# Optimization experiments

Hardware: AMD Instinct MI355X
Metric: run time of the kernel (lower is better)

The kernel has to match this reference:

```python
import jax, jax.numpy as jnp
import numpy as np

EMB = 384
HEADS = 6
QDIM = 64
DFF = 4 * EMB
EPS = 1e-5


def layer_norm(x, g, b):
    mu = jnp.mean(x, axis=-1, keepdims=True)
    var = jnp.mean((x - mu) ** 2, axis=-1, keepdims=True)
    return (x - mu) * jax.lax.rsqrt(var + EPS) * g + b


def setup_inputs() -> dict:
    key = jax.random.key(0)
    ks = jax.random.split(key, 12)
    s = EMB ** -0.5
    return {
        "x": jax.random.normal(ks[0], (32, 512, EMB), dtype=jnp.float32),
        "Wq": jax.random.normal(ks[1], (EMB, EMB), dtype=jnp.float32) * s,
        "Wk": jax.random.normal(ks[2], (EMB, EMB), dtype=jnp.float32) * s,
        "Wv": jax.random.normal(ks[3], (EMB, EMB), dtype=jnp.float32) * s,
        "Wp": jax.random.normal(ks[4], (EMB, EMB), dtype=jnp.float32) * s,
        "bp": jnp.zeros((EMB,), dtype=jnp.float32),
        "g1": jnp.ones((EMB,), dtype=jnp.float32),
        "b1": jnp.zeros((EMB,), dtype=jnp.float32),
        "g2": jnp.ones((EMB,), dtype=jnp.float32),
        "b2": jnp.zeros((EMB,), dtype=jnp.float32),
        "W1": jax.random.normal(ks[5], (EMB, DFF), dtype=jnp.float32) * s,
        "bf1": jnp.zeros((DFF,), dtype=jnp.float32),
        "W2": jax.random.normal(ks[6], (DFF, EMB), dtype=jnp.float32) * (DFF ** -0.5),
        "bf2": jnp.zeros((EMB,), dtype=jnp.float32),
    }


def reference(x, Wq, Wk, Wv, Wp, bp, g1, b1, g2, b2, W1, bf1, W2, bf2):
    B, T, C = x.shape
    # --- self-attention on ln1(x) ---
    h = layer_norm(x, g1, b1)
    q = (h @ Wq).reshape(B, T, HEADS, QDIM).transpose(0, 2, 1, 3)  # [B,H,T,D]
    k = (h @ Wk).reshape(B, T, HEADS, QDIM).transpose(0, 2, 1, 3)
    v = (h @ Wv).reshape(B, T, HEADS, QDIM).transpose(0, 2, 1, 3)
    aff = jnp.einsum('bhtd,bhsd->bhts', q, k) * (QDIM ** -0.5)  # [B,H,T,T]
    causal = jnp.tril(jnp.ones((T, T), dtype=bool))
    aff = jnp.where(causal, aff, -jnp.inf)
    aff = jax.nn.softmax(aff, axis=-1)
    o = jnp.einsum('bhts,bhsd->bhtd', aff, v)
    o = o.transpose(0, 2, 1, 3).reshape(B, T, C)
    x = x + (o @ Wp + bp)
    # --- feed-forward on ln2(x) ---
    h2 = layer_norm(x, g2, b2)
    ff = jax.nn.relu(h2 @ W1 + bf1) @ W2 + bf2
    return x + ff
```

## Files before the change

kernel.cpp:

```cpp
#include <hip/hip_runtime.h>
#include <cstdint>
#include <cstddef>

#define DEVINL __device__ __forceinline__

typedef short short8 __attribute__((ext_vector_type(8)));
typedef float f32x4 __attribute__((ext_vector_type(4)));
typedef unsigned short ushort;
typedef ushort u16x8 __attribute__((ext_vector_type(8)));
typedef ushort u16x4 __attribute__((ext_vector_type(4)));

DEVINL float bf2f(ushort u) {
  union { unsigned int i; float f; } v; v.i = ((unsigned int)u) << 16; return v.f;
}
DEVINL ushort f2bf(float f) {
  union { float f; unsigned int i; } v; v.f = f;
  unsigned int u = v.i;
  unsigned int r = u + 0x7fffu + ((u >> 16) & 1u);
  return (ushort)(r >> 16);
}

DEVINL void gl2lds16(const ushort* g, ushort* l) {
  __builtin_amdgcn_global_load_lds(
      (const __attribute__((address_space(1))) void*)g,
      (__attribute__((address_space(3))) void*)l, 16, 0, 0);
}

__global__ void transpose4_k(const float* __restrict__ i0, const float* __restrict__ i1,
                             const float* __restrict__ i2, const float* __restrict__ i3,
                             ushort* __restrict__ o0, ushort* __restrict__ o1,
                             ushort* __restrict__ o2, ushort* __restrict__ o3) {
  __shared__ float tile[32][33];
  int z = blockIdx.z;
  const float* in = (z == 0) ? i0 : (z == 1) ? i1 : (z == 2) ? i2 : i3;
  ushort* out = (z == 0) ? o0 : (z == 1) ? o1 : (z == 2) ? o2 : o3;
  int bx = blockIdx.x, by = blockIdx.y;
  int tx = threadIdx.x, ty = threadIdx.y;
  int x = bx * 32 + tx;
#pragma unroll
  for (int i = 0; i < 4; i++) {
    int y = by * 32 + ty + i * 8;
    tile[ty + i * 8][tx] = in[(size_t)y * 384 + x];
  }
  __syncthreads();
  int x2 = by * 32 + tx;
#pragma unroll
  for (int i = 0; i < 4; i++) {
    int y2 = bx * 32 + ty + i * 8;
    out[(size_t)y2 * 384 + x2] = f2bf(tile[tx][ty + i * 8]);
  }
}

__global__ void transpose_k(const float* __restrict__ in, ushort* __restrict__ out,
                            int R, int C) {
  __shared__ float tile[32][33];
  int bx = blockIdx.x, by = blockIdx.y;
  int tx = threadIdx.x, ty = threadIdx.y;
  int x = bx * 32 + tx;
#pragma unroll
  for (int i = 0; i < 4; i++) {
    int y = by * 32 + ty + i * 8;
    tile[ty + i * 8][tx] = in[(size_t)y * C + x];
  }
  __syncthreads();
  int x2 = by * 32 + tx;
#pragma unroll
  for (int i = 0; i < 4; i++) {
    int y2 = bx * 32 + ty + i * 8;
    out[(size_t)y2 * R + x2] = f2bf(tile[tx][ty + i * 8]);
  }
}

__global__ __launch_bounds__(256) void ln_k(const float* __restrict__ x,
                                            const float* __restrict__ g,
                                            const float* __restrict__ b,
                                            ushort* __restrict__ out) {
  int wave = threadIdx.x >> 6;
  int lane = threadIdx.x & 63;
  int row = blockIdx.x * 4 + wave;
  const float* xr = x + (size_t)row * 384;
  float v[6];
#pragma unroll
  for (int j = 0; j < 3; j++) {
    float2 p = *(const float2*)(xr + lane * 2 + j * 128);
    v[2 * j] = p.x;
    v[2 * j + 1] = p.y;
  }
  float s = v[0] + v[1] + v[2] + v[3] + v[4] + v[5];
#pragma unroll
  for (int off = 32; off; off >>= 1) s += __shfl_xor(s, off);
  float mu = s * (1.0f / 384.0f);
  float s2 = 0.f;
#pragma unroll
  for (int j = 0; j < 6; j++) { float d = v[j] - mu; s2 += d * d; }
#pragma unroll
  for (int off = 32; off; off >>= 1) s2 += __shfl_xor(s2, off);
  float rs = rsqrtf(s2 * (1.0f / 384.0f) + 1e-5f);
  ushort* orow = out + (size_t)row * 384;
#pragma unroll
  for (int j = 0; j < 3; j++) {
    int c = lane * 2 + j * 128;
    float2 pg = *(const float2*)(g + c);
    float2 pb = *(const float2*)(b + c);
    float y0 = (v[2 * j] - mu) * rs * pg.x + pb.x;
    float y1 = (v[2 * j + 1] - mu) * rs * pg.y + pb.y;
    uint32_t po = (uint32_t)f2bf(y0) | ((uint32_t)f2bf(y1) << 16);
    *(uint32_t*)(orow + c) = po;
  }
}

template <int MODE, int TN>
__global__ __launch_bounds__(256) void gemm_k(
    const ushort* __restrict__ A, int K,
    const ushort* __restrict__ WTa, const ushort* __restrict__ WTb,
    const ushort* __restrict__ WTc,
    const float* __restrict__ bias, const float* residf,
    ushort* __restrict__ outa, ushort* __restrict__ outb,
    ushort* __restrict__ outc, float* outf) {
  constexpr int NJ = TN / 32;
  __shared__ __align__(16) ushort As[128 * 32];
  __shared__ __align__(16) ushort Bs[TN * 32];
  int tid = threadIdx.x;
  int lane = tid & 63, wave = tid >> 6;
  int wm = wave & 1, wn = wave >> 1;
  int q4 = lane >> 4, ln16 = lane & 15;
  int rowBase = blockIdx.x * 128;
  int colBase = blockIdx.y * TN;

  const ushort* WT;
  if (MODE == 0) {
    int z = blockIdx.z;
    WT = (z == 0) ? WTa : (z == 1) ? WTb : WTc;
  } else {
    WT = WTa;
  }

  f32x4 acc[4][NJ];
#pragma unroll
  for (int i = 0; i < 4; i++)
#pragma unroll
    for (int j = 0; j < NJ; j++) acc[i][j] = (f32x4){0.f, 0.f, 0.f, 0.f};

  int lr = lane >> 2;
  int chunk = (lane & 3) ^ (lr & 3);
  int rslot = (q4 ^ (ln16 & 3)) << 3;

  for (int kb = 0; kb < K; kb += 32) {
#pragma unroll
    for (int h = 0; h < 128; h += 64) {
      int base = wave * 16 + h;
      gl2lds16(&A[(size_t)(rowBase + base + lr) * K + kb + chunk * 8], &As[base * 32]);
    }
#pragma unroll
    for (int h = 0; h < TN; h += 64) {
      int base = wave * 16 + h;
      gl2lds16(&WT[(size_t)(colBase + base + lr) * K + kb + chunk * 8], &Bs[base * 32]);
    }
    __syncthreads();
    short8 af[4], bfr[NJ];
#pragma unroll
    for (int i = 0; i < 4; i++) {
      int ar = wm * 64 + i * 16 + ln16;
      af[i] = *(const short8*)&As[ar * 32 + rslot];
    }
#pragma unroll
    for (int j = 0; j < NJ; j++) {
      int br = wn * (TN / 2) + j * 16 + ln16;
      bfr[j] = *(const short8*)&Bs[br * 32 + rslot];
    }
#pragma unroll
    for (int i = 0; i < 4; i++)
#pragma unroll
      for (int j = 0; j < NJ; j++)
        acc[i][j] = __builtin_amdgcn_mfma_f32_16x16x32_bf16(af[i], bfr[j], acc[i][j], 0, 0, 0);
    __syncthreads();
  }

#pragma unroll
  for (int i = 0; i < 4; i++) {
#pragma unroll
    for (int j = 0; j < NJ; j++) {
      int row0 = rowBase + wm * 64 + i * 16 + q4 * 4;
      int col = colBase + wn * (TN / 2) + j * 16 + ln16;
      if (MODE == 0) {
        int z = blockIdx.z;
        if (z < 2) {
          ushort* o = (z == 0) ? outa : outb;
#pragma unroll
          for (int r = 0; r < 4; r++) {
            int row = row0 + r;
            int bb = row >> 9, t = row & 511, h = col >> 6, d = col & 63;
            o[(((size_t)(bb * 6 + h) * 512) + t) * 64 + d] = f2bf(acc[i][j][r]);
          }
        } else {
          int bb = row0 >> 9, t0 = row0 & 511, h = col >> 6, d = col & 63;
          u16x4 pk = {f2bf(acc[i][j][0]), f2bf(acc[i][j][1]), f2bf(acc[i][j][2]),
                      f2bf(acc[i][j][3])};
          *(u16x4*)&outc[(((size_t)(bb * 6 + h) * 64) + d) * 512 + t0] = pk;
        }
      } else if (MODE == 1) {
        float bcol = bias[col];
#pragma unroll
        for (int r = 0; r < 4; r++) {
          size_t idx = (size_t)(row0 + r) * 384 + col;
          outf[idx] = acc[i][j][r] + bcol + residf[idx];
        }
      } else {
        float bcol = bias[col];
#pragma unroll
        for (int r = 0; r < 4; r++) {
          size_t idx = (size_t)(row0 + r) * 1536 + col;
          float vv = acc[i][j][r] + bcol;
          outa[idx] = f2bf(vv > 0.f ? vv : 0.f);
        }
      }
    }
  }
}

__global__ __launch_bounds__(256) void attn_k(const ushort* __restrict__ qg,
                                              const ushort* __restrict__ kg,
                                              const ushort* __restrict__ vtg,
                                              ushort* __restrict__ outg) {
  __shared__ ushort Ks[64][88];
  __shared__ ushort VTs[64][88];
  __shared__ ushort Pw[4][16][88];
  int tid = threadIdx.x, lane = tid & 63, wave = tid >> 6;
  int qb = blockIdx.x;
  int bh = blockIdx.y;
  int quad = lane >> 4, ln16 = lane & 15;
  int q0 = qb * 64 + wave * 16;
  int t_row = q0 + ln16;

  const ushort* qp = qg + (size_t)bh * 512 * 64;
  const ushort* kp = kg + (size_t)bh * 512 * 64;
  const ushort* vp = vtg + (size_t)bh * 64 * 512;

  short8 bq0 = *(const short8*)&qp[(size_t)t_row * 64 + quad * 8];
  short8 bq1 = *(const short8*)&qp[(size_t)t_row * 64 + 32 + quad * 8];

  f32x4 O[4];
#pragma unroll
  for (int dt = 0; dt < 4; dt++) O[dt] = (f32x4){0.f, 0.f, 0.f, 0.f};
  float m_ = -3.0e38f, l_ = 0.f;

  const float SC = 0.125f * 1.44269504088896f;

  for (int s0 = 0; s0 <= qb * 64; s0 += 64) {
    {
      int r = tid >> 2;
      int c0 = (tid & 3) * 8;
#pragma unroll
      for (int p = 0; p < 2; p++) {
        int c = c0 + p * 32;
        *(u16x8*)&Ks[r][c] = *(const u16x8*)&kp[(size_t)(s0 + r) * 64 + c];
        *(u16x8*)&VTs[r][c] = *(const u16x8*)&vp[(size_t)r * 512 + s0 + c];
      }
    }
    __syncthreads();

    f32x4 St[4];
#pragma unroll
    for (int kt = 0; kt < 4; kt++) {
      short8 a0 = *(const short8*)&Ks[kt * 16 + ln16][quad * 8];
      short8 a1 = *(const short8*)&Ks[kt * 16 + ln16][32 + quad * 8];
      f32x4 z = (f32x4){0.f, 0.f, 0.f, 0.f};
      z = __builtin_amdgcn_mfma_f32_16x16x32_bf16(a0, bq0, z, 0, 0, 0);
      z = __builtin_amdgcn_mfma_f32_16x16x32_bf16(a1, bq1, z, 0, 0, 0);
      St[kt] = z;
    }
#pragma unroll
    for (int kt = 0; kt < 4; kt++)
#pragma unroll
      for (int r = 0; r < 4; r++) {
        int s_abs = s0 + kt * 16 + quad * 4 + r;
        float vv = St[kt][r] * SC;
        St[kt][r] = (s_abs <= t_row) ? vv : -3.0e38f;
      }
    float vm = St[0][0];
#pragma unroll
    for (int kt = 0; kt < 4; kt++)
#pragma unroll
      for (int r = 0; r < 4; r++) vm = fmaxf(vm, St[kt][r]);
    vm = fmaxf(vm, __shfl_xor(vm, 16));
    vm = fmaxf(vm, __shfl_xor(vm, 32));
    float mn = fmaxf(m_, vm);
    float alpha = exp2f(m_ - mn);
    m_ = mn;
    float ps = 0.f;
#pragma unroll
    for (int kt = 0; kt < 4; kt++)
#pragma unroll
      for (int r = 0; r < 4; r++) {
        float p = exp2f(St[kt][r] - mn);
        St[kt][r] = p;
        ps += p;
      }
    ps += __shfl_xor(ps, 16);
    ps += __shfl_xor(ps, 32);
    l_ = l_ * alpha + ps;
#pragma unroll
    for (int dt = 0; dt < 4; dt++)
#pragma unroll
      for (int r = 0; r < 4; r++) O[dt][r] *= alpha;

#pragma unroll
    for (int kt = 0; kt < 4; kt++) {
      u16x4 pk = {f2bf(St[kt][0]), f2bf(St[kt][1]), f2bf(St[kt][2]), f2bf(St[kt][3])};
      *(u16x4*)&Pw[wave][ln16][kt * 16 + quad * 4] = pk;
    }
    asm volatile("" ::: "memory");
    union { u16x8 u; short8 s; } p0, p1;
    p0.u = *(const u16x8*)&Pw[wave][ln16][quad * 8];
    p1.u = *(const u16x8*)&Pw[wave][ln16][32 + quad * 8];
#pragma unroll
    for (int dt = 0; dt < 4; dt++) {
      short8 v0 = *(const short8*)&VTs[dt * 16 + ln16][quad * 8];
      short8 v1 = *(const short8*)&VTs[dt * 16 + ln16][32 + quad * 8];
      O[dt] = __builtin_amdgcn_mfma_f32_16x16x32_bf16(v0, p0.s, O[dt], 0, 0, 0);
      O[dt] = __builtin_amdgcn_mfma_f32_16x16x32_bf16(v1, p1.s, O[dt], 0, 0, 0);
    }
    __syncthreads();
  }

  float inv = 1.0f / l_;
  int b = bh / 6, h = bh % 6;
  size_t rowbase = ((size_t)(b * 512) + t_row) * 384 + h * 64;
#pragma unroll
  for (int dt = 0; dt < 4; dt++) {
    u16x4 pk = {f2bf(O[dt][0] * inv), f2bf(O[dt][1] * inv), f2bf(O[dt][2] * inv),
                f2bf(O[dt][3] * inv)};
    *(u16x4*)&outg[rowbase + dt * 16 + quad * 4] = pk;
  }
}

extern "C" void kernel_launch(void* const* d_in, const int* in_sizes, int n_in,
                              void* d_out, int out_size, void* d_ws, size_t ws_size,
                              hipStream_t stream) {
  const float* x = (const float*)d_in[0];
  const float* Wq = (const float*)d_in[1];
  const float* Wk = (const float*)d_in[2];
  const float* Wv = (const float*)d_in[3];
  const float* Wp = (const float*)d_in[4];
  const float* bp = (const float*)d_in[5];
  const float* g1 = (const float*)d_in[6];
  const float* b1 = (const float*)d_in[7];
  const float* g2 = (const float*)d_in[8];
  const float* b2 = (const float*)d_in[9];
  const float* W1 = (const float*)d_in[10];
  const float* bf1 = (const float*)d_in[11];
  const float* W2 = (const float*)d_in[12];
  const float* bf2 = (const float*)d_in[13];
  float* outp = (float*)d_out;

  char* ws = (char*)d_ws;
  size_t off = 0;
  auto alloc = [&](size_t elems) {
    ushort* p = (ushort*)(ws + off);
    off += elems * 2;
    return p;
  };
  ushort* WqT = alloc((size_t)384 * 384);
  ushort* WkT = alloc((size_t)384 * 384);
  ushort* WvT = alloc((size_t)384 * 384);
  ushort* WpT = alloc((size_t)384 * 384);
  ushort* W1T = alloc((size_t)384 * 1536);
  ushort* W2T = alloc((size_t)1536 * 384);
  ushort* bufq = alloc((size_t)16384 * 384);
  ushort* m1 = alloc((size_t)16384 * 1536);
  ushort* h1_attn = m1;
  ushort* bufk = m1 + (size_t)16384 * 384;
  ushort* vT = m1 + (size_t)2 * 16384 * 384;

  dim3 tb(32, 8);
  transpose4_k<<<dim3(12, 12, 4), tb, 0, stream>>>(Wq, Wk, Wv, Wp, WqT, WkT, WvT, WpT);
  transpose_k<<<dim3(48, 12), tb, 0, stream>>>(W1, W1T, 384, 1536);
  transpose_k<<<dim3(12, 48), tb, 0, stream>>>(W2, W2T, 1536, 384);

  ln_k<<<4096, 256, 0, stream>>>(x, g1, b1, h1_attn);
  gemm_k<0, 128><<<dim3(128, 3, 3), 256, 0, stream>>>(
      h1_attn, 384, WqT, WkT, WvT, nullptr, nullptr, bufq, bufk, vT, nullptr);
  attn_k<<<dim3(8, 192), 256, 0, stream>>>(bufq, bufk, vT, h1_attn);
  gemm_k<1, 64><<<dim3(128, 6), 256, 0, stream>>>(
      h1_attn, 384, WpT, nullptr, nullptr, bp, x, nullptr, nullptr, nullptr, outp);
  ln_k<<<4096, 256, 0, stream>>>(outp, g2, b2, bufq);
  gemm_k<2, 128><<<dim3(128, 12), 256, 0, stream>>>(
      bufq, 384, W1T, nullptr, nullptr, bf1, nullptr, m1, nullptr, nullptr, nullptr);
  gemm_k<1, 64><<<dim3(128, 6), 256, 0, stream>>>(
      m1, 1536, W2T, nullptr, nullptr, bf2, outp, nullptr, nullptr, nullptr, outp);
}
```

Baseline: 280.8 us.

## Pair causal query tiles per block and map heads to XCDs for balance

Each attention block now handles two query tiles, lo=pr and hi=7-pr, so every block does the same total causal work. The K/V tiles loaded into LDS are shared between both tiles, which halves K/V staging for the low tile. The grid is flattened to 768 blocks, and block indices are mapped so that all blocks for a given batch-head land on the same XCD, aiming for L2 reuse of K/V. The cost is higher register pressure from two accumulator sets and half as many blocks.

```diff
diff --git a/kernel.cpp b/kernel.cpp
--- a/kernel.cpp
+++ b/kernel.cpp
@@ -226,47 +226,44 @@
   __shared__ ushort VTs[64][88];
   __shared__ ushort Pw[4][16][88];
   int tid = threadIdx.x, lane = tid & 63, wave = tid >> 6;
-  int qb = blockIdx.x;
-  int bh = blockIdx.y;
+  int l = blockIdx.x;
+  int xcd = l & 7, m = l >> 3;
+  int bh = xcd * 24 + (m >> 2);
+  int pr = m & 3;
+  int lo = pr, hi = 7 - pr;
   int quad = lane >> 4, ln16 = lane & 15;
-  int q0 = qb * 64 + wave * 16;
-  int t_row = q0 + ln16;
 
   const ushort* qp = qg + (size_t)bh * 512 * 64;
   const ushort* kp = kg + (size_t)bh * 512 * 64;
   const ushort* vp = vtg + (size_t)bh * 64 * 512;
 
-  short8 bq0 = *(const short8*)&qp[(size_t)t_row * 64 + quad * 8];
-  short8 bq1 = *(const short8*)&qp[(size_t)t_row * 64 + 32 + quad * 8];
-
-  f32x4 O[4];
-#pragma unroll
-  for (int dt = 0; dt < 4; dt++) O[dt] = (f32x4){0.f, 0.f, 0.f, 0.f};
-  float m_ = -3.0e38f, l_ = 0.f;
+  int t_lo = lo * 64 + wave * 16 + ln16;
+  int t_hi = hi * 64 + wave * 16 + ln16;
+  short8 bqlo0 = *(const short8*)&qp[(size_t)t_lo * 64 + quad * 8];
+  short8 bqlo1 = *(const short8*)&qp[(size_t)t_lo * 64 + 32 + quad * 8];
+  short8 bqhi0 = *(const short8*)&qp[(size_t)t_hi * 64 + quad * 8];
+  short8 bqhi1 = *(const short8*)&qp[(size_t)t_hi * 64 + 32 + quad * 8];
+
+  f32x4 Olo[4], Ohi[4];
+#pragma unroll
+  for (int dt = 0; dt < 4; dt++) {
+    Olo[dt] = (f32x4){0.f, 0.f, 0.f, 0.f};
+    Ohi[dt] = (f32x4){0.f, 0.f, 0.f, 0.f};
+  }
+  float m_lo = -3.0e38f, l_lo = 0.f, m_hi = -3.0e38f, l_hi = 0.f;
 
   const float SC = 0.125f * 1.44269504088896f;
 
-  for (int s0 = 0; s0 <= qb * 64; s0 += 64) {
-    {
-      int r = tid >> 2;
-      int c0 = (tid & 3) * 8;
-#pragma unroll
-      for (int p = 0; p < 2; p++) {
-        int c = c0 + p * 32;
-        *(u16x8*)&Ks[r][c] = *(const u16x8*)&kp[(size_t)(s0 + r) * 64 + c];
-        *(u16x8*)&VTs[r][c] = *(const u16x8*)&vp[(size_t)r * 512 + s0 + c];
-      }
-    }
-    __syncthreads();
-
+  auto process = [&](short8 q0f, short8 q1f, int t_row, float& m_, float& l_,
+                     f32x4* O, int s0) {
     f32x4 St[4];
 #pragma unroll
     for (int kt = 0; kt < 4; kt++) {
       short8 a0 = *(const short8*)&Ks[kt * 16 + ln16][quad * 8];
       short8 a1 = *(const short8*)&Ks[kt * 16 + ln16][32 + quad * 8];
       f32x4 z = (f32x4){0.f, 0.f, 0.f, 0.f};
-      z = __builtin_amdgcn_mfma_f32_16x16x32_bf16(a0, bq0, z, 0, 0, 0);
-      z = __builtin_amdgcn_mfma_f32_16x16x32_bf16(a1, bq1, z, 0, 0, 0);
+      z = __builtin_amdgcn_mfma_f32_16x16x32_bf16(a0, q0f, z, 0, 0, 0);
+      z = __builtin_amdgcn_mfma_f32_16x16x32_bf16(a1, q1f, z, 0, 0, 0);
       St[kt] = z;
     }
 #pragma unroll
@@ -304,6 +301,7 @@
 #pragma unroll
       for (int r = 0; r < 4; r++) O[dt][r] *= alpha;
 
+    asm volatile("" ::: "memory");
 #pragma unroll
     for (int kt = 0; kt < 4; kt++) {
       u16x4 pk = {f2bf(St[kt][0]), f2bf(St[kt][1]), f2bf(St[kt][2]), f2bf(St[kt][3])};
@@ -320,17 +318,37 @@
       O[dt] = __builtin_amdgcn_mfma_f32_16x16x32_bf16(v0, p0.s, O[dt], 0, 0, 0);
       O[dt] = __builtin_amdgcn_mfma_f32_16x16x32_bf16(v1, p1.s, O[dt], 0, 0, 0);
     }
+  };
+
+  for (int s0 = 0; s0 <= hi * 64; s0 += 64) {
+    {
+      int r = tid >> 2;
+      int c0 = (tid & 3) * 8;
+#pragma unroll
+      for (int p = 0; p < 2; p++) {
+        int c = c0 + p * 32;
+        *(u16x8*)&Ks[r][c] = *(const u16x8*)&kp[(size_t)(s0 + r) * 64 + c];
+        *(u16x8*)&VTs[r][c] = *(const u16x8*)&vp[(size_t)r * 512 + s0 + c];
+      }
+    }
     __syncthreads();
-  }
-
-  float inv = 1.0f / l_;
+    if (s0 <= lo * 64) process(bqlo0, bqlo1, t_lo, m_lo, l_lo, Olo, s0);
+    process(bqhi0, bqhi1, t_hi, m_hi, l_hi, Ohi, s0);
+    __syncthreads();
+  }
+
   int b = bh / 6, h = bh % 6;
-  size_t rowbase = ((size_t)(b * 512) + t_row) * 384 + h * 64;
+  float ilo = 1.0f / l_lo, ihi = 1.0f / l_hi;
+  size_t base_lo = ((size_t)(b * 512) + t_lo) * 384 + h * 64;
+  size_t base_hi = ((size_t)(b * 512) + t_hi) * 384 + h * 64;
 #pragma unroll
   for (int dt = 0; dt < 4; dt++) {
-    u16x4 pk = {f2bf(O[dt][0] * inv), f2bf(O[dt][1] * inv), f2bf(O[dt][2] * inv),
-                f2bf(O[dt][3] * inv)};
-    *(u16x4*)&outg[rowbase + dt * 16 + quad * 4] = pk;
+    u16x4 plo = {f2bf(Olo[dt][0] * ilo), f2bf(Olo[dt][1] * ilo),
+                 f2bf(Olo[dt][2] * ilo), f2bf(Olo[dt][3] * ilo)};
+    *(u16x4*)&outg[base_lo + dt * 16 + quad * 4] = plo;
+    u16x4 phi = {f2bf(Ohi[dt][0] * ihi), f2bf(Ohi[dt][1] * ihi),
+                 f2bf(Ohi[dt][2] * ihi), f2bf(Ohi[dt][3] * ihi)};
+    *(u16x4*)&outg[base_hi + dt * 16 + quad * 4] = phi;
   }
 }
 
@@ -380,7 +398,7 @@
   ln_k<<<4096, 256, 0, stream>>>(x, g1, b1, h1_attn);
   gemm_k<0, 128><<<dim3(128, 3, 3), 256, 0, stream>>>(
       h1_attn, 384, WqT, WkT, WvT, nullptr, nullptr, bufq, bufk, vT, nullptr);
-  attn_k<<<dim3(8, 192), 256, 0, stream>>>(bufq, bufk, vT, h1_attn);
+  attn_k<<<768, 256, 0, stream>>>(bufq, bufk, vT, h1_attn);
   gemm_k<1, 64><<<dim3(128, 6), 256, 0, stream>>>(
       h1_attn, 384, WpT, nullptr, nullptr, bp, x, nullptr, nullptr, nullptr, outp);
   ln_k<<<4096, 256, 0, stream>>>(outp, g2, b2, bufq);
```

Measured after the change: 276.3 us. About the same (-1.6%).
